# Kernel tuning notes

Measured on AMD Instinct MI355X. Metric: run time of the kernel, lower is better.

## Reference

```python
import jax, jax.numpy as jnp
import numpy as np

DROPOUT_P = 0.1


def setup_inputs() -> dict:
    key = jax.random.key(0)
    kq, kk, kv, km = jax.random.split(key, 4)
    B, H, S, D = 8, 16, 1024, 64
    query = jax.random.normal(kq, (B, H, S, D), dtype=jnp.float32)
    key_t = jax.random.normal(kk, (B, H, S, D), dtype=jnp.float32)
    value = jax.random.normal(kv, (B, H, S, D), dtype=jnp.float32)
    mask = jax.random.randint(km, (B, 1, S, S), 0, 2, dtype=jnp.int32)
    return {"query": query, "key": key_t, "value": value, "mask": mask}


def reference(query, key, value, mask):
    d_k = query.shape[-1]
    # scores: [B, H, S, S]
    scores = jnp.einsum("bhqd,bhkd->bhqk", query, key) / jnp.sqrt(
        jnp.asarray(d_k, dtype=query.dtype)
    )
    scores = jnp.where(mask == 0, jnp.asarray(-jnp.inf, dtype=scores.dtype), scores)
    attn_weights = jax.nn.softmax(scores, axis=-1)
    # deterministic dropout (train-mode semantics, fixed RNG)
    drop_key = jax.random.fold_in(jax.random.key(42), 7)
    keep = jax.random.bernoulli(drop_key, 1.0 - DROPOUT_P, attn_weights.shape)
    attn_weights = jnp.where(keep, attn_weights / (1.0 - DROPOUT_P), 0.0)
    output = jnp.einsum("bhqk,bhkd->bhqd", attn_weights, value)
    return (output, attn_weights)
```

## Files before the change

### kernel.cpp

```cpp
#include <hip/hip_runtime.h>


constexpr int Bc = 8, Hc = 16, Sc = 1024, Dc = 64;
constexpr int TQ  = 8;
constexpr int WTP = 12;

typedef float v4f __attribute__((ext_vector_type(4)));

#define TF_ROUND(x0, x1, r) { x0 += x1; x1 = ((x1 << (r)) | (x1 >> (32 - (r)))); x1 ^= x0; }

__host__ __device__ __forceinline__ void threefry2x32(unsigned k0, unsigned k1,
                                                      unsigned x0, unsigned x1,
                                                      unsigned& o0, unsigned& o1) {
  const unsigned k2 = k0 ^ k1 ^ 0x1BD11BDAu;
  x0 += k0; x1 += k1;
  TF_ROUND(x0, x1, 13) TF_ROUND(x0, x1, 15) TF_ROUND(x0, x1, 26) TF_ROUND(x0, x1, 6)
  x0 += k1; x1 += k2 + 1u;
  TF_ROUND(x0, x1, 17) TF_ROUND(x0, x1, 29) TF_ROUND(x0, x1, 16) TF_ROUND(x0, x1, 24)
  x0 += k2; x1 += k0 + 2u;
  TF_ROUND(x0, x1, 13) TF_ROUND(x0, x1, 15) TF_ROUND(x0, x1, 26) TF_ROUND(x0, x1, 6)
  x0 += k0; x1 += k1 + 3u;
  TF_ROUND(x0, x1, 17) TF_ROUND(x0, x1, 29) TF_ROUND(x0, x1, 16) TF_ROUND(x0, x1, 24)
  x0 += k1; x1 += k2 + 4u;
  TF_ROUND(x0, x1, 13) TF_ROUND(x0, x1, 15) TF_ROUND(x0, x1, 26) TF_ROUND(x0, x1, 6)
  x0 += k2; x1 += k0 + 5u;
  o0 = x0; o1 = x1;
}

__global__ __launch_bounds__(256, 3)
void attn_fused(const float* __restrict__ Qg, const float* __restrict__ Kg,
                const float* __restrict__ Vg, const int* __restrict__ Mg,
                float* __restrict__ Og, float* __restrict__ Ag,
                unsigned key0, unsigned key1)
{
  __shared__ __align__(16) float WT[Sc][WTP];
  __shared__ float REDm[4][8];
  __shared__ float REDs[4][8];

  const int tid = threadIdx.x;
  const int w   = tid >> 6;
  const int l   = tid & 63;
  const int h   = blockIdx.y;
  const int b   = blockIdx.z;
  const int q0  = blockIdx.x * TQ;
  const size_t bh = (size_t)b * Hc + h;

  const float* __restrict__ Kb = Kg + bh * Sc * Dc;
  const float* __restrict__ Vb = Vg + bh * Sc * Dc;
  const float* __restrict__ Qb = Qg + bh * Sc * Dc + (size_t)q0 * Dc;

  #pragma unroll 1
  for (int kb = 0; kb < 4; ++kb) {
    const int k = kb * 256 + w * 64 + l;
    const float4* __restrict__ Krow = (const float4*)(Kb + (size_t)k * Dc);
    float4 kr[16];
    #pragma unroll
    for (int j = 0; j < 16; ++j) kr[j] = Krow[j];
    float acc[8];
    #pragma unroll
    for (int q = 0; q < 8; ++q) {
      const float4* __restrict__ Qrow = (const float4*)(Qb + q * Dc);
      float a = 0.f;
      #pragma unroll
      for (int j = 0; j < 16; ++j) {
        const float4 qv = Qrow[j];
        a = fmaf(kr[j].x, qv.x, a);
        a = fmaf(kr[j].y, qv.y, a);
        a = fmaf(kr[j].z, qv.z, a);
        a = fmaf(kr[j].w, qv.w, a);
      }
      acc[q] = a * 0.125f;
    }
    *(float4*)&WT[k][0] = make_float4(acc[0], acc[1], acc[2], acc[3]);
    *(float4*)&WT[k][4] = make_float4(acc[4], acc[5], acc[6], acc[7]);
  }

  const float NEG = -__builtin_inff();
  float sv[4][8];
  #pragma unroll
  for (int kb = 0; kb < 4; ++kb) {
    const int k = kb * 256 + w * 64 + l;
    const float4 lo = *(const float4*)&WT[k][0];
    const float4 hi = *(const float4*)&WT[k][4];
    sv[kb][0] = lo.x; sv[kb][1] = lo.y; sv[kb][2] = lo.z; sv[kb][3] = lo.w;
    sv[kb][4] = hi.x; sv[kb][5] = hi.y; sv[kb][6] = hi.z; sv[kb][7] = hi.w;
    const int* __restrict__ mcol = Mg + (size_t)b * Sc * Sc + k;
    #pragma unroll
    for (int q = 0; q < 8; ++q)
      if (mcol[(size_t)(q0 + q) * Sc] == 0) sv[kb][q] = NEG;
  }

  float mx[8];
  #pragma unroll
  for (int q = 0; q < 8; ++q) {
    float m = fmaxf(fmaxf(sv[0][q], sv[1][q]), fmaxf(sv[2][q], sv[3][q]));
    #pragma unroll
    for (int off = 32; off > 0; off >>= 1) m = fmaxf(m, __shfl_xor(m, off));
    if (l == 0) REDm[w][q] = m;
  }
  __syncthreads();
  #pragma unroll
  for (int q = 0; q < 8; ++q)
    mx[q] = fmaxf(fmaxf(REDm[0][q], REDm[1][q]), fmaxf(REDm[2][q], REDm[3][q]));

  #pragma unroll
  for (int kb = 0; kb < 4; ++kb)
    #pragma unroll
    for (int q = 0; q < 8; ++q)
      sv[kb][q] = __expf(sv[kb][q] - mx[q]);
  #pragma unroll
  for (int q = 0; q < 8; ++q) {
    float s = (sv[0][q] + sv[1][q]) + (sv[2][q] + sv[3][q]);
    #pragma unroll
    for (int off = 32; off > 0; off >>= 1) s += __shfl_xor(s, off);
    if (l == 0) REDs[w][q] = s;
  }
  __syncthreads();
  float inv9[8];
  #pragma unroll
  for (int q = 0; q < 8; ++q)
    inv9[q] = 1.0f / (((REDs[0][q] + REDs[1][q]) + (REDs[2][q] + REDs[3][q])) * 0.9f);

  unsigned keep = 0u;
  const unsigned ibase = ((unsigned)(((unsigned)b * Hc + h) * Sc + q0)) * (unsigned)Sc
                         + (unsigned)(w * 64 + l);
  #pragma unroll 8
  for (int t2 = 0; t2 < 32; ++t2) {
    const int kb = t2 >> 3, q = t2 & 7;
    unsigned o0, o1;
    threefry2x32(key0, key1, 0u, ibase + (unsigned)(q * Sc + kb * 256), o0, o1);
    const unsigned bits = o0 ^ o1;
    const float u = __uint_as_float((bits >> 9) | 0x3f800000u) - 1.0f;
    keep |= (u < 0.9f) ? (1u << t2) : 0u;
  }

  float* __restrict__ Arow = Ag + bh * (size_t)Sc * Sc + (size_t)q0 * Sc;
  #pragma unroll
  for (int kb = 0; kb < 4; ++kb) {
    const int k = kb * 256 + w * 64 + l;
    float wv[8];
    #pragma unroll
    for (int q = 0; q < 8; ++q) {
      wv[q] = ((keep >> (kb * 8 + q)) & 1u) ? sv[kb][q] * inv9[q] : 0.f;
      __builtin_nontemporal_store(wv[q], &Arow[(size_t)q * Sc + k]);
    }
    *(float4*)&WT[k][0] = make_float4(wv[0], wv[1], wv[2], wv[3]);
    *(float4*)&WT[k][4] = make_float4(wv[4], wv[5], wv[6], wv[7]);
  }
  __syncthreads();

  const int ks = tid & 15;
  const int dq = tid >> 4;
  float4 acc[8];
  #pragma unroll
  for (int q = 0; q < 8; ++q) acc[q] = make_float4(0.f, 0.f, 0.f, 0.f);

  #pragma unroll 2
  for (int i = 0; i < 64; ++i) {
    const int k = i * 16 + ks;
    const float4 vv = *(const float4*)(Vb + (size_t)k * Dc + dq * 4);
    const float4 lo = *(const float4*)&WT[k][0];
    const float4 hi = *(const float4*)&WT[k][4];
#define ACCQ(qi, wq) { acc[qi].x = fmaf(wq, vv.x, acc[qi].x); \
                       acc[qi].y = fmaf(wq, vv.y, acc[qi].y); \
                       acc[qi].z = fmaf(wq, vv.z, acc[qi].z); \
                       acc[qi].w = fmaf(wq, vv.w, acc[qi].w); }
    ACCQ(0, lo.x) ACCQ(1, lo.y) ACCQ(2, lo.z) ACCQ(3, lo.w)
    ACCQ(4, hi.x) ACCQ(5, hi.y) ACCQ(6, hi.z) ACCQ(7, hi.w)
#undef ACCQ
  }

  #pragma unroll
  for (int off = 1; off <= 8; off <<= 1) {
    #pragma unroll
    for (int q = 0; q < 8; ++q) {
      acc[q].x += __shfl_xor(acc[q].x, off);
      acc[q].y += __shfl_xor(acc[q].y, off);
      acc[q].z += __shfl_xor(acc[q].z, off);
      acc[q].w += __shfl_xor(acc[q].w, off);
    }
  }
  if ((l & 15) == 0) {
    float* __restrict__ Obase = Og + bh * (size_t)Sc * Dc + (size_t)q0 * Dc + dq * 4;
    #pragma unroll
    for (int q = 0; q < 8; ++q) {
      const v4f t = { acc[q].x, acc[q].y, acc[q].z, acc[q].w };
      __builtin_nontemporal_store(t, (v4f*)(Obase + (size_t)q * Dc));
    }
  }
}

extern "C" void kernel_launch(void* const* d_in, const int* in_sizes, int n_in,
                              void* d_out, int out_size, void* d_ws, size_t ws_size,
                              hipStream_t stream) {
  const float* Qg = (const float*)d_in[0];
  const float* Kg = (const float*)d_in[1];
  const float* Vg = (const float*)d_in[2];
  const int*   Mg = (const int*)d_in[3];
  float* Og = (float*)d_out;
  float* Ag = Og + (size_t)Bc * Hc * Sc * Dc;

  unsigned k0, k1;
  threefry2x32(0u, 42u, 0u, 7u, k0, k1);

  dim3 grid(Sc / TQ, Hc, Bc);
  attn_fused<<<grid, 256, 0, stream>>>(Qg, Kg, Vg, Mg, Og, Ag, k0, k1);
}
```

Baseline: 1.862 ms.

## Halve LDS staging buffer, keep scores in registers, raise occupancy to six blocks

Scores are now accumulated in registers across a loop over D slices instead of being written to shared memory and read back, which removes one LDS round trip. The mask is loaded up front and packed into a bitmask, and the PV stage stages weights through a half-size LDS buffer in two passes. Shared memory per block drops by half, so launch bounds move from 3 to 6 blocks per CU. The cost is an extra barrier and tighter register limits that could cause spills with 32 scores live per thread.

```diff
diff --git a/kernel.cpp b/kernel.cpp
--- a/kernel.cpp
+++ b/kernel.cpp
@@ -27,19 +27,20 @@
   o0 = x0; o1 = x1;
 }
 
-__global__ __launch_bounds__(256, 3)
+__global__ __launch_bounds__(256, 6)
 void attn_fused(const float* __restrict__ Qg, const float* __restrict__ Kg,
                 const float* __restrict__ Vg, const int* __restrict__ Mg,
                 float* __restrict__ Og, float* __restrict__ Ag,
                 unsigned key0, unsigned key1)
 {
-  __shared__ __align__(16) float WT[Sc][WTP];
+  __shared__ __align__(16) float WTh[512][WTP];
   __shared__ float REDm[4][8];
   __shared__ float REDs[4][8];
 
   const int tid = threadIdx.x;
   const int w   = tid >> 6;
   const int l   = tid & 63;
+  const int kl  = w * 64 + l;
   const int h   = blockIdx.y;
   const int b   = blockIdx.z;
   const int q0  = blockIdx.x * TQ;
@@ -49,81 +50,9 @@
   const float* __restrict__ Vb = Vg + bh * Sc * Dc;
   const float* __restrict__ Qb = Qg + bh * Sc * Dc + (size_t)q0 * Dc;
 
-  #pragma unroll 1
-  for (int kb = 0; kb < 4; ++kb) {
-    const int k = kb * 256 + w * 64 + l;
-    const float4* __restrict__ Krow = (const float4*)(Kb + (size_t)k * Dc);
-    float4 kr[16];
-    #pragma unroll
-    for (int j = 0; j < 16; ++j) kr[j] = Krow[j];
-    float acc[8];
-    #pragma unroll
-    for (int q = 0; q < 8; ++q) {
-      const float4* __restrict__ Qrow = (const float4*)(Qb + q * Dc);
-      float a = 0.f;
-      #pragma unroll
-      for (int j = 0; j < 16; ++j) {
-        const float4 qv = Qrow[j];
-        a = fmaf(kr[j].x, qv.x, a);
-        a = fmaf(kr[j].y, qv.y, a);
-        a = fmaf(kr[j].z, qv.z, a);
-        a = fmaf(kr[j].w, qv.w, a);
-      }
-      acc[q] = a * 0.125f;
-    }
-    *(float4*)&WT[k][0] = make_float4(acc[0], acc[1], acc[2], acc[3]);
-    *(float4*)&WT[k][4] = make_float4(acc[4], acc[5], acc[6], acc[7]);
-  }
-
-  const float NEG = -__builtin_inff();
-  float sv[4][8];
-  #pragma unroll
-  for (int kb = 0; kb < 4; ++kb) {
-    const int k = kb * 256 + w * 64 + l;
-    const float4 lo = *(const float4*)&WT[k][0];
-    const float4 hi = *(const float4*)&WT[k][4];
-    sv[kb][0] = lo.x; sv[kb][1] = lo.y; sv[kb][2] = lo.z; sv[kb][3] = lo.w;
-    sv[kb][4] = hi.x; sv[kb][5] = hi.y; sv[kb][6] = hi.z; sv[kb][7] = hi.w;
-    const int* __restrict__ mcol = Mg + (size_t)b * Sc * Sc + k;
-    #pragma unroll
-    for (int q = 0; q < 8; ++q)
-      if (mcol[(size_t)(q0 + q) * Sc] == 0) sv[kb][q] = NEG;
-  }
-
-  float mx[8];
-  #pragma unroll
-  for (int q = 0; q < 8; ++q) {
-    float m = fmaxf(fmaxf(sv[0][q], sv[1][q]), fmaxf(sv[2][q], sv[3][q]));
-    #pragma unroll
-    for (int off = 32; off > 0; off >>= 1) m = fmaxf(m, __shfl_xor(m, off));
-    if (l == 0) REDm[w][q] = m;
-  }
-  __syncthreads();
-  #pragma unroll
-  for (int q = 0; q < 8; ++q)
-    mx[q] = fmaxf(fmaxf(REDm[0][q], REDm[1][q]), fmaxf(REDm[2][q], REDm[3][q]));
-
-  #pragma unroll
-  for (int kb = 0; kb < 4; ++kb)
-    #pragma unroll
-    for (int q = 0; q < 8; ++q)
-      sv[kb][q] = __expf(sv[kb][q] - mx[q]);
-  #pragma unroll
-  for (int q = 0; q < 8; ++q) {
-    float s = (sv[0][q] + sv[1][q]) + (sv[2][q] + sv[3][q]);
-    #pragma unroll
-    for (int off = 32; off > 0; off >>= 1) s += __shfl_xor(s, off);
-    if (l == 0) REDs[w][q] = s;
-  }
-  __syncthreads();
-  float inv9[8];
-  #pragma unroll
-  for (int q = 0; q < 8; ++q)
-    inv9[q] = 1.0f / (((REDs[0][q] + REDs[1][q]) + (REDs[2][q] + REDs[3][q])) * 0.9f);
-
   unsigned keep = 0u;
-  const unsigned ibase = ((unsigned)(((unsigned)b * Hc + h) * Sc + q0)) * (unsigned)Sc
-                         + (unsigned)(w * 64 + l);
+  const unsigned ibase = ((unsigned)((b * Hc + h) * Sc + q0)) * (unsigned)Sc
+                         + (unsigned)kl;
   #pragma unroll 8
   for (int t2 = 0; t2 < 32; ++t2) {
     const int kb = t2 >> 3, q = t2 & 7;
@@ -134,20 +63,90 @@
     keep |= (u < 0.9f) ? (1u << t2) : 0u;
   }
 
-  float* __restrict__ Arow = Ag + bh * (size_t)Sc * Sc + (size_t)q0 * Sc;
-  #pragma unroll
-  for (int kb = 0; kb < 4; ++kb) {
-    const int k = kb * 256 + w * 64 + l;
-    float wv[8];
-    #pragma unroll
-    for (int q = 0; q < 8; ++q) {
-      wv[q] = ((keep >> (kb * 8 + q)) & 1u) ? sv[kb][q] * inv9[q] : 0.f;
-      __builtin_nontemporal_store(wv[q], &Arow[(size_t)q * Sc + k]);
-    }
-    *(float4*)&WT[k][0] = make_float4(wv[0], wv[1], wv[2], wv[3]);
-    *(float4*)&WT[k][4] = make_float4(wv[4], wv[5], wv[6], wv[7]);
+  unsigned mbits = 0u;
+  {
+    const int* __restrict__ mc = Mg + (size_t)b * Sc * Sc + (size_t)q0 * Sc + kl;
+    #pragma unroll
+    for (int kb = 0; kb < 4; ++kb)
+      #pragma unroll
+      for (int q = 0; q < 8; ++q)
+        mbits |= (mc[(size_t)q * Sc + kb * 256] != 0) ? (1u << (kb * 8 + q)) : 0u;
+  }
+
+  float sv[4][8];
+  #pragma unroll
+  for (int kb = 0; kb < 4; ++kb)
+    #pragma unroll
+    for (int q = 0; q < 8; ++q) sv[kb][q] = 0.f;
+
+  #pragma unroll 1
+  for (int ds = 0; ds < 16; ++ds) {
+    float4 qv[8];
+    #pragma unroll
+    for (int q = 0; q < 8; ++q)
+      qv[q] = *(const float4*)(Qb + (size_t)q * Dc + ds * 4);
+    #pragma unroll
+    for (int kb = 0; kb < 4; ++kb) {
+      const float4 kv = *(const float4*)(Kb + (size_t)(kb * 256 + kl) * Dc + ds * 4);
+      #pragma unroll
+      for (int q = 0; q < 8; ++q) {
+        sv[kb][q] = fmaf(kv.x, qv[q].x, sv[kb][q]);
+        sv[kb][q] = fmaf(kv.y, qv[q].y, sv[kb][q]);
+        sv[kb][q] = fmaf(kv.z, qv[q].z, sv[kb][q]);
+        sv[kb][q] = fmaf(kv.w, qv[q].w, sv[kb][q]);
+      }
+    }
+  }
+
+  const float NEG = -__builtin_inff();
+  #pragma unroll
+  for (int kb = 0; kb < 4; ++kb)
+    #pragma unroll
+    for (int q = 0; q < 8; ++q) {
+      const float s = sv[kb][q] * 0.125f;
+      sv[kb][q] = ((mbits >> (kb * 8 + q)) & 1u) ? s : NEG;
+    }
+
+  float mx[8];
+  #pragma unroll
+  for (int q = 0; q < 8; ++q) {
+    float m = fmaxf(fmaxf(sv[0][q], sv[1][q]), fmaxf(sv[2][q], sv[3][q]));
+    #pragma unroll
+    for (int off = 32; off > 0; off >>= 1) m = fmaxf(m, __shfl_xor(m, off));
+    if (l == 0) REDm[w][q] = m;
   }
   __syncthreads();
+  #pragma unroll
+  for (int q = 0; q < 8; ++q)
+    mx[q] = fmaxf(fmaxf(REDm[0][q], REDm[1][q]), fmaxf(REDm[2][q], REDm[3][q]));
+
+  #pragma unroll
+  for (int kb = 0; kb < 4; ++kb)
+    #pragma unroll
+    for (int q = 0; q < 8; ++q)
+      sv[kb][q] = __expf(sv[kb][q] - mx[q]);
+  #pragma unroll
+  for (int q = 0; q < 8; ++q) {
+    float s = (sv[0][q] + sv[1][q]) + (sv[2][q] + sv[3][q]);
+    #pragma unroll
+    for (int off = 32; off > 0; off >>= 1) s += __shfl_xor(s, off);
+    if (l == 0) REDs[w][q] = s;
+  }
+  __syncthreads();
+  float inv9[8];
+  #pragma unroll
+  for (int q = 0; q < 8; ++q)
+    inv9[q] = 1.0f / (((REDs[0][q] + REDs[1][q]) + (REDs[2][q] + REDs[3][q])) * 0.9f);
+
+  float* __restrict__ Arow = Ag + bh * (size_t)Sc * Sc + (size_t)q0 * Sc + kl;
+  #pragma unroll
+  for (int kb = 0; kb < 4; ++kb)
+    #pragma unroll
+    for (int q = 0; q < 8; ++q) {
+      const float wv = ((keep >> (kb * 8 + q)) & 1u) ? sv[kb][q] * inv9[q] : 0.f;
+      sv[kb][q] = wv;
+      __builtin_nontemporal_store(wv, &Arow[(size_t)q * Sc + kb * 256]);
+    }
 
   const int ks = tid & 15;
   const int dq = tid >> 4;
@@ -155,19 +154,33 @@
   #pragma unroll
   for (int q = 0; q < 8; ++q) acc[q] = make_float4(0.f, 0.f, 0.f, 0.f);
 
-  #pragma unroll 2
-  for (int i = 0; i < 64; ++i) {
-    const int k = i * 16 + ks;
-    const float4 vv = *(const float4*)(Vb + (size_t)k * Dc + dq * 4);
-    const float4 lo = *(const float4*)&WT[k][0];
-    const float4 hi = *(const float4*)&WT[k][4];
+  #pragma unroll 1
+  for (int half = 0; half < 2; ++half) {
+    if (half) __syncthreads();
+    #pragma unroll
+    for (int kk = 0; kk < 2; ++kk) {
+      const int kb = half * 2 + kk;
+      const int kr = kk * 256 + kl;
+      *(float4*)&WTh[kr][0] = make_float4(sv[kb][0], sv[kb][1], sv[kb][2], sv[kb][3]);
+      *(float4*)&WTh[kr][4] = make_float4(sv[kb][4], sv[kb][5], sv[kb][6], sv[kb][7]);
+    }
+    __syncthreads();
+
+    #pragma unroll 4
+    for (int i = 0; i < 32; ++i) {
+      const int kr = i * 16 + ks;
+      const int k  = half * 512 + kr;
+      const float4 vv = *(const float4*)(Vb + (size_t)k * Dc + dq * 4);
+      const float4 lo = *(const float4*)&WTh[kr][0];
+      const float4 hi = *(const float4*)&WTh[kr][4];
 #define ACCQ(qi, wq) { acc[qi].x = fmaf(wq, vv.x, acc[qi].x); \
                        acc[qi].y = fmaf(wq, vv.y, acc[qi].y); \
                        acc[qi].z = fmaf(wq, vv.z, acc[qi].z); \
                        acc[qi].w = fmaf(wq, vv.w, acc[qi].w); }
-    ACCQ(0, lo.x) ACCQ(1, lo.y) ACCQ(2, lo.z) ACCQ(3, lo.w)
-    ACCQ(4, hi.x) ACCQ(5, hi.y) ACCQ(6, hi.z) ACCQ(7, hi.w)
+      ACCQ(0, lo.x) ACCQ(1, lo.y) ACCQ(2, lo.z) ACCQ(3, lo.w)
+      ACCQ(4, hi.x) ACCQ(5, hi.y) ACCQ(6, hi.z) ACCQ(7, hi.w)
 #undef ACCQ
+    }
   }
 
   #pragma unroll
```

New measurement: 2.451 ms. 1.32x slower.

## Remap blocks per XCD, prefetch mask bits, and hoist dropout RNG early

Applied to the files above, without the earlier changes.

The launch becomes a 1D grid with a swizzle that gives consecutive workgroup ids sharing the same (b,h) to the same XCD (orig&7). The goal is better per-XCD L2 reuse of K and V. Mask values are now loaded up front into a bitmask, and the threefry dropout bits are computed before the QK^T loop, so the latency of those global loads can overlap with ALU work. The PV loop unroll also goes from 2 to 4. The extra live registers may reduce occupancy at launch_bounds(256,3).

```diff
diff --git a/kernel.cpp b/kernel.cpp
--- a/kernel.cpp
+++ b/kernel.cpp
@@ -37,21 +37,47 @@
   __shared__ float REDm[4][8];
   __shared__ float REDs[4][8];
 
+  const unsigned orig = blockIdx.x;
+  const unsigned wg   = (orig & 7u) * 2048u + (orig >> 3);
+  const int q0 = (int)(wg & 127u) * TQ;
+  const int h  = (int)(wg >> 7) & 15;
+  const int b  = (int)(wg >> 11);
+
   const int tid = threadIdx.x;
   const int w   = tid >> 6;
   const int l   = tid & 63;
-  const int h   = blockIdx.y;
-  const int b   = blockIdx.z;
-  const int q0  = blockIdx.x * TQ;
   const size_t bh = (size_t)b * Hc + h;
 
   const float* __restrict__ Kb = Kg + bh * Sc * Dc;
   const float* __restrict__ Vb = Vg + bh * Sc * Dc;
   const float* __restrict__ Qb = Qg + bh * Sc * Dc + (size_t)q0 * Dc;
 
+  unsigned mbits = 0u;
+  {
+    const int* __restrict__ mc = Mg + (size_t)b * Sc * Sc + (size_t)q0 * Sc + tid;
+    #pragma unroll
+    for (int kb = 0; kb < 4; ++kb)
+      #pragma unroll
+      for (int q = 0; q < 8; ++q)
+        mbits |= (mc[(size_t)q * Sc + kb * 256] != 0) ? (1u << (kb * 8 + q)) : 0u;
+  }
+
+  unsigned keep = 0u;
+  const unsigned ibase = ((unsigned)((b * Hc + h) * Sc + q0)) * (unsigned)Sc
+                         + (unsigned)tid;
+  #pragma unroll 8
+  for (int t2 = 0; t2 < 32; ++t2) {
+    const int kb = t2 >> 3, q = t2 & 7;
+    unsigned o0, o1;
+    threefry2x32(key0, key1, 0u, ibase + (unsigned)(q * Sc + kb * 256), o0, o1);
+    const unsigned bits = o0 ^ o1;
+    const float u = __uint_as_float((bits >> 9) | 0x3f800000u) - 1.0f;
+    keep |= (u < 0.9f) ? (1u << t2) : 0u;
+  }
+
   #pragma unroll 1
   for (int kb = 0; kb < 4; ++kb) {
-    const int k = kb * 256 + w * 64 + l;
+    const int k = kb * 256 + tid;
     const float4* __restrict__ Krow = (const float4*)(Kb + (size_t)k * Dc);
     float4 kr[16];
     #pragma unroll
@@ -59,7 +85,7 @@
     float acc[8];
     #pragma unroll
     for (int q = 0; q < 8; ++q) {
-      const float4* __restrict__ Qrow = (const float4*)(Qb + q * Dc);
+      const float4* __restrict__ Qrow = (const float4*)(Qb + (size_t)q * Dc);
       float a = 0.f;
       #pragma unroll
       for (int j = 0; j < 16; ++j) {
@@ -79,15 +105,14 @@
   float sv[4][8];
   #pragma unroll
   for (int kb = 0; kb < 4; ++kb) {
-    const int k = kb * 256 + w * 64 + l;
+    const int k = kb * 256 + tid;
     const float4 lo = *(const float4*)&WT[k][0];
     const float4 hi = *(const float4*)&WT[k][4];
     sv[kb][0] = lo.x; sv[kb][1] = lo.y; sv[kb][2] = lo.z; sv[kb][3] = lo.w;
     sv[kb][4] = hi.x; sv[kb][5] = hi.y; sv[kb][6] = hi.z; sv[kb][7] = hi.w;
-    const int* __restrict__ mcol = Mg + (size_t)b * Sc * Sc + k;
     #pragma unroll
     for (int q = 0; q < 8; ++q)
-      if (mcol[(size_t)(q0 + q) * Sc] == 0) sv[kb][q] = NEG;
+      if (!((mbits >> (kb * 8 + q)) & 1u)) sv[kb][q] = NEG;
   }
 
   float mx[8];
@@ -121,28 +146,15 @@
   for (int q = 0; q < 8; ++q)
     inv9[q] = 1.0f / (((REDs[0][q] + REDs[1][q]) + (REDs[2][q] + REDs[3][q])) * 0.9f);
 
-  unsigned keep = 0u;
-  const unsigned ibase = ((unsigned)(((unsigned)b * Hc + h) * Sc + q0)) * (unsigned)Sc
-                         + (unsigned)(w * 64 + l);
-  #pragma unroll 8
-  for (int t2 = 0; t2 < 32; ++t2) {
-    const int kb = t2 >> 3, q = t2 & 7;
-    unsigned o0, o1;
-    threefry2x32(key0, key1, 0u, ibase + (unsigned)(q * Sc + kb * 256), o0, o1);
-    const unsigned bits = o0 ^ o1;
-    const float u = __uint_as_float((bits >> 9) | 0x3f800000u) - 1.0f;
-    keep |= (u < 0.9f) ? (1u << t2) : 0u;
-  }
-
-  float* __restrict__ Arow = Ag + bh * (size_t)Sc * Sc + (size_t)q0 * Sc;
+  float* __restrict__ Arow = Ag + bh * (size_t)Sc * Sc + (size_t)q0 * Sc + tid;
   #pragma unroll
   for (int kb = 0; kb < 4; ++kb) {
-    const int k = kb * 256 + w * 64 + l;
+    const int k = kb * 256 + tid;
     float wv[8];
     #pragma unroll
     for (int q = 0; q < 8; ++q) {
       wv[q] = ((keep >> (kb * 8 + q)) & 1u) ? sv[kb][q] * inv9[q] : 0.f;
-      __builtin_nontemporal_store(wv[q], &Arow[(size_t)q * Sc + k]);
+      __builtin_nontemporal_store(wv[q], &Arow[(size_t)q * Sc + kb * 256]);
     }
     *(float4*)&WT[k][0] = make_float4(wv[0], wv[1], wv[2], wv[3]);
     *(float4*)&WT[k][4] = make_float4(wv[4], wv[5], wv[6], wv[7]);
@@ -155,7 +167,7 @@
   #pragma unroll
   for (int q = 0; q < 8; ++q) acc[q] = make_float4(0.f, 0.f, 0.f, 0.f);
 
-  #pragma unroll 2
+  #pragma unroll 4
   for (int i = 0; i < 64; ++i) {
     const int k = i * 16 + ks;
     const float4 vv = *(const float4*)(Vb + (size_t)k * Dc + dq * 4);
@@ -203,6 +215,5 @@
   unsigned k0, k1;
   threefry2x32(0u, 42u, 0u, 7u, k0, k1);
 
-  dim3 grid(Sc / TQ, Hc, Bc);
-  attn_fused<<<grid, 256, 0, stream>>>(Qg, Kg, Vg, Mg, Og, Ag, k0, k1);
+  attn_fused<<<dim3(16384), 256, 0, stream>>>(Qg, Kg, Vg, Mg, Og, Ag, k0, k1);
 }
```

Measured after the change: 1.720 ms. 7.6% less time.
